# Optimization experiments

Hardware: AMD Instinct MI355X
Metric: run time of the kernel (lower is better)

The kernel has to match this reference:

```python
import jax, jax.numpy as jnp
import numpy as np

TEMPERATURE = 0.2
HYPER_GAMMA = 0.5
EPS = 1e-12  # torch F.normalize / cosine_similarity eps guard (1e-12 / 1e-8)

def setup_inputs() -> dict:
    key = jax.random.key(0)
    k1, k2 = jax.random.split(key)
    B, D = 4096, 1024
    return {
        "emb_i": jax.random.normal(k1, (B, D), dtype=jnp.float32),
        "emb_j": jax.random.normal(k2, (B, D), dtype=jnp.float32),
    }

def _l2_normalize(x, eps=EPS):
    n = jnp.sqrt(jnp.sum(x * x, axis=1, keepdims=True))
    return x / jnp.maximum(n, eps)

def reference(emb_i, emb_j):
    B = emb_i.shape[0]
    z_i = _l2_normalize(emb_i)
    z_j = _l2_normalize(emb_j)
    # cosine similarity of unit vectors == dot product; sim[a, b] = <z_j[a], z_i[b]>
    sim = jnp.einsum('ad,bd->ab', z_j, z_i)  # [B, B]
    sim_positive = jnp.diagonal(sim)
    positives_exp = jnp.exp(-sim_positive + TEMPERATURE)
    neg_mask = 1.0 - jnp.eye(B, dtype=sim.dtype)
    negatives_exp = neg_mask * jnp.exp(sim - TEMPERATURE)
    positives_sum = jnp.sum(jnp.log1p(positives_exp)) / B
    negatives_sum = jnp.sum(jnp.log1p(negatives_exp)) / (B * (B - 1))
    return HYPER_GAMMA * positives_sum + (1.0 - HYPER_GAMMA) * negatives_sum
```

## Files before the change

### kernel.cpp

```cpp
#include <hip/hip_runtime.h>
#include <math.h>

#define B_ROWS 4096
#define D_DIM  1024
static constexpr float TEMP = 0.2f;

typedef __attribute__((ext_vector_type(8))) short bf16x8;
typedef __attribute__((ext_vector_type(4))) float f32x4;

__device__ inline unsigned short f2bf(float f) {
    unsigned int u = __float_as_uint(f);
    u += 0x7fffu + ((u >> 16) & 1u);
    return (unsigned short)(u >> 16);
}

__device__ inline void gload_lds16(const unsigned short* g, unsigned short* l) {
    __builtin_amdgcn_global_load_lds(
        (const __attribute__((address_space(1))) unsigned int*)g,
        (__attribute__((address_space(3))) unsigned int*)l,
        16, 0, 0);
}


__global__ void init_acc_kernel(float* __restrict__ w) {
    w[0] = 0.0f;
    w[1] = 0.0f;
}

__global__ __launch_bounds__(256) void norm_cast_kernel(
        const float* __restrict__ emb_i, const float* __restrict__ emb_j,
        unsigned short* __restrict__ Zi, unsigned short* __restrict__ Zj) {
    const int row = blockIdx.x;
    const float* src;
    unsigned short* dst;
    int r;
    if (row < B_ROWS) { src = emb_i; dst = Zi; r = row; }
    else              { src = emb_j; dst = Zj; r = row - B_ROWS; }

    const int t = threadIdx.x;
    const float4* p = (const float4*)(src + (size_t)r * D_DIM);
    float4 v = p[t];
    float s = v.x * v.x + v.y * v.y + v.z * v.z + v.w * v.w;
    #pragma unroll
    for (int off = 32; off > 0; off >>= 1) s += __shfl_down(s, off, 64);
    __shared__ float ls[4];
    __shared__ float invn;
    if ((t & 63) == 0) ls[t >> 6] = s;
    __syncthreads();
    if (t == 0) {
        float tot = ls[0] + ls[1] + ls[2] + ls[3];
        invn = 1.0f / fmaxf(sqrtf(tot), 1e-12f);
    }
    __syncthreads();
    const float inv = invn;
    ushort4 o;
    o.x = f2bf(v.x * inv); o.y = f2bf(v.y * inv);
    o.z = f2bf(v.z * inv); o.w = f2bf(v.w * inv);
    ((ushort4*)(dst + (size_t)r * D_DIM))[t] = o;
}

__global__ __launch_bounds__(256) void simloss_mfma_kernel(
        const unsigned short* __restrict__ Zi,
        const unsigned short* __restrict__ Zj,
        float* __restrict__ w) {
    __shared__ __align__(16) unsigned short lA[128 * 32];
    __shared__ __align__(16) unsigned short lB[128 * 32];
    __shared__ float rn[4], rp[4];

    const int tid  = threadIdx.x;
    const int lane = tid & 63;
    const int wave = tid >> 6;
    const int wy = wave >> 1, wx = wave & 1;

    const int rowBase = blockIdx.y * 128;
    const int colBase = blockIdx.x * 128;

    const int c0 = 2 * wave, c1 = c0 + 1;
    const int srow  = lane >> 2;
    const int skoff = (lane & 3) * 8;
    const unsigned short* gA0 = Zj + (size_t)(rowBase + 16 * c0 + srow) * D_DIM + skoff;
    const unsigned short* gA1 = Zj + (size_t)(rowBase + 16 * c1 + srow) * D_DIM + skoff;
    const unsigned short* gB0 = Zi + (size_t)(colBase + 16 * c0 + srow) * D_DIM + skoff;
    const unsigned short* gB1 = Zi + (size_t)(colBase + 16 * c1 + srow) * D_DIM + skoff;
    unsigned short* sA0 = lA + c0 * 512;
    unsigned short* sA1 = lA + c1 * 512;
    unsigned short* sB0 = lB + c0 * 512;
    unsigned short* sB1 = lB + c1 * 512;

    const unsigned short* fA = lA + ((wy * 64 + (lane & 15)) * 32 + (lane >> 4) * 8);
    const unsigned short* fB = lB + ((wx * 64 + (lane & 15)) * 32 + (lane >> 4) * 8);

    f32x4 acc[4][4];
    #pragma unroll
    for (int i = 0; i < 4; ++i)
        #pragma unroll
        for (int j = 0; j < 4; ++j)
            acc[i][j] = (f32x4){0.f, 0.f, 0.f, 0.f};

    for (int k0 = 0; k0 < D_DIM; k0 += 32) {
        __syncthreads();
        gload_lds16(gA0, sA0);
        gload_lds16(gA1, sA1);
        gload_lds16(gB0, sB0);
        gload_lds16(gB1, sB1);
        gA0 += 32; gA1 += 32; gB0 += 32; gB1 += 32;
        __syncthreads();

        bf16x8 af[4], bf[4];
        #pragma unroll
        for (int i = 0; i < 4; ++i) af[i] = *(const bf16x8*)(fA + i * 16 * 32);
        #pragma unroll
        for (int j = 0; j < 4; ++j) bf[j] = *(const bf16x8*)(fB + j * 16 * 32);
        #pragma unroll
        for (int i = 0; i < 4; ++i)
            #pragma unroll
            for (int j = 0; j < 4; ++j)
                acc[i][j] = __builtin_amdgcn_mfma_f32_16x16x32_bf16(
                    af[i], bf[j], acc[i][j], 0, 0, 0);
    }

    const int cr = (lane >> 4) * 4;
    const int cc = lane & 15;
    float neg = 0.f, pos = 0.f;
    #pragma unroll
    for (int i = 0; i < 4; ++i) {
        const int abase = rowBase + wy * 64 + i * 16 + cr;
        #pragma unroll
        for (int j = 0; j < 4; ++j) {
            const int b = colBase + wx * 64 + j * 16 + cc;
            #pragma unroll
            for (int r = 0; r < 4; ++r) {
                const float x = acc[i][j][r] - TEMP;
                if (abase + r == b) pos += __logf(1.0f + __expf(-x));
                else                neg += __logf(1.0f + __expf(x));
            }
        }
    }

    #pragma unroll
    for (int off = 32; off > 0; off >>= 1) {
        neg += __shfl_down(neg, off, 64);
        pos += __shfl_down(pos, off, 64);
    }
    if (lane == 0) { rn[wave] = neg; rp[wave] = pos; }
    __syncthreads();
    if (tid == 0) {
        atomicAdd(&w[1], rn[0] + rn[1] + rn[2] + rn[3]);
        if (blockIdx.x == blockIdx.y)
            atomicAdd(&w[0], rp[0] + rp[1] + rp[2] + rp[3]);
    }
}

__global__ void finalize_kernel(const float* __restrict__ w, float* __restrict__ out) {
    const float pos = w[0] / (float)B_ROWS;
    const float neg = w[1] / ((float)B_ROWS * (float)(B_ROWS - 1));
    out[0] = 0.5f * pos + 0.5f * neg;
}

extern "C" void kernel_launch(void* const* d_in, const int* in_sizes, int n_in,
                              void* d_out, int out_size, void* d_ws, size_t ws_size,
                              hipStream_t stream) {
    const float* emb_i = (const float*)d_in[0];
    const float* emb_j = (const float*)d_in[1];
    float* w = (float*)d_ws;
    unsigned short* Zi = (unsigned short*)(w + 16);
    unsigned short* Zj = Zi + (size_t)B_ROWS * D_DIM;
    float* out = (float*)d_out;

    init_acc_kernel<<<1, 1, 0, stream>>>(w);
    norm_cast_kernel<<<2 * B_ROWS, 256, 0, stream>>>(emb_i, emb_j, Zi, Zj);
    dim3 grid(B_ROWS / 128, B_ROWS / 128);
    simloss_mfma_kernel<<<grid, 256, 0, stream>>>(Zi, Zj, w);
    finalize_kernel<<<1, 1, 0, stream>>>(w, out);
}
```

Before: 137.5 us.

## Fuse init/finalize kernels, widen K-tile with swizzled LDS, wave-per-row normalize

```diff
diff --git a/kernel.cpp b/kernel.cpp
--- a/kernel.cpp
+++ b/kernel.cpp
@@ -22,73 +22,69 @@
 }
 
 
-__global__ void init_acc_kernel(float* __restrict__ w) {
-    w[0] = 0.0f;
-    w[1] = 0.0f;
-}
-
 __global__ __launch_bounds__(256) void norm_cast_kernel(
         const float* __restrict__ emb_i, const float* __restrict__ emb_j,
-        unsigned short* __restrict__ Zi, unsigned short* __restrict__ Zj) {
-    const int row = blockIdx.x;
-    const float* src;
-    unsigned short* dst;
-    int r;
+        unsigned short* __restrict__ Zi, unsigned short* __restrict__ Zj,
+        float* __restrict__ w) {
+    const int tid = threadIdx.x;
+    if (blockIdx.x == 0 && tid == 0) {
+        w[0] = 0.0f; w[1] = 0.0f;
+        ((unsigned int*)w)[2] = 0u;
+    }
+    const int wave = tid >> 6, lane = tid & 63;
+    const int row = blockIdx.x * 4 + wave;
+    const float* src; unsigned short* dst; int r;
     if (row < B_ROWS) { src = emb_i; dst = Zi; r = row; }
     else              { src = emb_j; dst = Zj; r = row - B_ROWS; }
 
-    const int t = threadIdx.x;
     const float4* p = (const float4*)(src + (size_t)r * D_DIM);
-    float4 v = p[t];
-    float s = v.x * v.x + v.y * v.y + v.z * v.z + v.w * v.w;
+    float4 v0 = p[lane], v1 = p[64 + lane], v2 = p[128 + lane], v3 = p[192 + lane];
+    float s = v0.x*v0.x + v0.y*v0.y + v0.z*v0.z + v0.w*v0.w
+            + v1.x*v1.x + v1.y*v1.y + v1.z*v1.z + v1.w*v1.w
+            + v2.x*v2.x + v2.y*v2.y + v2.z*v2.z + v2.w*v2.w
+            + v3.x*v3.x + v3.y*v3.y + v3.z*v3.z + v3.w*v3.w;
     #pragma unroll
-    for (int off = 32; off > 0; off >>= 1) s += __shfl_down(s, off, 64);
-    __shared__ float ls[4];
-    __shared__ float invn;
-    if ((t & 63) == 0) ls[t >> 6] = s;
-    __syncthreads();
-    if (t == 0) {
-        float tot = ls[0] + ls[1] + ls[2] + ls[3];
-        invn = 1.0f / fmaxf(sqrtf(tot), 1e-12f);
-    }
-    __syncthreads();
-    const float inv = invn;
-    ushort4 o;
-    o.x = f2bf(v.x * inv); o.y = f2bf(v.y * inv);
-    o.z = f2bf(v.z * inv); o.w = f2bf(v.w * inv);
-    ((ushort4*)(dst + (size_t)r * D_DIM))[t] = o;
+    for (int m = 1; m < 64; m <<= 1) s += __shfl_xor(s, m, 64);
+    const float inv = 1.0f / fmaxf(sqrtf(s), 1e-12f);
+
+    ushort4* q = (ushort4*)(dst + (size_t)r * D_DIM);
+    ushort4 o0 = { f2bf(v0.x*inv), f2bf(v0.y*inv), f2bf(v0.z*inv), f2bf(v0.w*inv) };
+    ushort4 o1 = { f2bf(v1.x*inv), f2bf(v1.y*inv), f2bf(v1.z*inv), f2bf(v1.w*inv) };
+    ushort4 o2 = { f2bf(v2.x*inv), f2bf(v2.y*inv), f2bf(v2.z*inv), f2bf(v2.w*inv) };
+    ushort4 o3 = { f2bf(v3.x*inv), f2bf(v3.y*inv), f2bf(v3.z*inv), f2bf(v3.w*inv) };
+    q[lane] = o0; q[64 + lane] = o1; q[128 + lane] = o2; q[192 + lane] = o3;
 }
 
-__global__ __launch_bounds__(256) void simloss_mfma_kernel(
+__global__ __launch_bounds__(256, 4) void simloss_mfma_kernel(
         const unsigned short* __restrict__ Zi,
         const unsigned short* __restrict__ Zj,
-        float* __restrict__ w) {
-    __shared__ __align__(16) unsigned short lA[128 * 32];
-    __shared__ __align__(16) unsigned short lB[128 * 32];
+        float* __restrict__ w, float* __restrict__ out) {
+    __shared__ __align__(16) unsigned short lA[128 * 64];
+    __shared__ __align__(16) unsigned short lB[128 * 64];
     __shared__ float rn[4], rp[4];
 
     const int tid  = threadIdx.x;
     const int lane = tid & 63;
     const int wave = tid >> 6;
     const int wy = wave >> 1, wx = wave & 1;
-
     const int rowBase = blockIdx.y * 128;
     const int colBase = blockIdx.x * 128;
 
-    const int c0 = 2 * wave, c1 = c0 + 1;
-    const int srow  = lane >> 2;
-    const int skoff = (lane & 3) * 8;
-    const unsigned short* gA0 = Zj + (size_t)(rowBase + 16 * c0 + srow) * D_DIM + skoff;
-    const unsigned short* gA1 = Zj + (size_t)(rowBase + 16 * c1 + srow) * D_DIM + skoff;
-    const unsigned short* gB0 = Zi + (size_t)(colBase + 16 * c0 + srow) * D_DIM + skoff;
-    const unsigned short* gB1 = Zi + (size_t)(colBase + 16 * c1 + srow) * D_DIM + skoff;
-    unsigned short* sA0 = lA + c0 * 512;
-    unsigned short* sA1 = lA + c1 * 512;
-    unsigned short* sB0 = lB + c0 * 512;
-    unsigned short* sB1 = lB + c1 * 512;
+    const int lrow = lane >> 3;
+    const int lp   = lane & 7;
+    const int lc   = (lp - lrow) & 7;
+    const unsigned short* gA = Zj + (size_t)(rowBase + wave * 32 + lrow) * D_DIM + lc * 8;
+    const unsigned short* gB = Zi + (size_t)(colBase + wave * 32 + lrow) * D_DIM + lc * 8;
+    unsigned short* sA = lA + wave * 4 * 512;
+    unsigned short* sB = lB + wave * 4 * 512;
 
-    const unsigned short* fA = lA + ((wy * 64 + (lane & 15)) * 32 + (lane >> 4) * 8);
-    const unsigned short* fB = lB + ((wx * 64 + (lane & 15)) * 32 + (lane >> 4) * 8);
+    const int fr = lane & 15;
+    const int p0 = ((lane >> 4) + (lane & 7)) & 7;
+    const int p1 = (p0 + 4) & 7;
+    const unsigned short* fA0 = lA + (wy * 64 + fr) * 64 + p0 * 8;
+    const unsigned short* fA1 = lA + (wy * 64 + fr) * 64 + p1 * 8;
+    const unsigned short* fB0 = lB + (wx * 64 + fr) * 64 + p0 * 8;
+    const unsigned short* fB1 = lB + (wx * 64 + fr) * 64 + p1 * 8;
 
     f32x4 acc[4][4];
     #pragma unroll
@@ -97,26 +93,37 @@
         for (int j = 0; j < 4; ++j)
             acc[i][j] = (f32x4){0.f, 0.f, 0.f, 0.f};
 
-    for (int k0 = 0; k0 < D_DIM; k0 += 32) {
+    for (int k0 = 0; k0 < D_DIM; k0 += 64) {
         __syncthreads();
-        gload_lds16(gA0, sA0);
-        gload_lds16(gA1, sA1);
-        gload_lds16(gB0, sB0);
-        gload_lds16(gB1, sB1);
-        gA0 += 32; gA1 += 32; gB0 += 32; gB1 += 32;
+        #pragma unroll
+        for (int ch = 0; ch < 4; ++ch) {
+            gload_lds16(gA + ch * 8 * D_DIM, sA + ch * 512);
+            gload_lds16(gB + ch * 8 * D_DIM, sB + ch * 512);
+        }
+        gA += 64; gB += 64;
         __syncthreads();
 
-        bf16x8 af[4], bf[4];
+        bf16x8 a[4], b[4];
         #pragma unroll
-        for (int i = 0; i < 4; ++i) af[i] = *(const bf16x8*)(fA + i * 16 * 32);
+        for (int i = 0; i < 4; ++i) a[i] = *(const bf16x8*)(fA0 + i * 1024);
         #pragma unroll
-        for (int j = 0; j < 4; ++j) bf[j] = *(const bf16x8*)(fB + j * 16 * 32);
+        for (int j = 0; j < 4; ++j) b[j] = *(const bf16x8*)(fB0 + j * 1024);
         #pragma unroll
         for (int i = 0; i < 4; ++i)
             #pragma unroll
             for (int j = 0; j < 4; ++j)
                 acc[i][j] = __builtin_amdgcn_mfma_f32_16x16x32_bf16(
-                    af[i], bf[j], acc[i][j], 0, 0, 0);
+                    a[i], b[j], acc[i][j], 0, 0, 0);
+        #pragma unroll
+        for (int i = 0; i < 4; ++i) a[i] = *(const bf16x8*)(fA1 + i * 1024);
+        #pragma unroll
+        for (int j = 0; j < 4; ++j) b[j] = *(const bf16x8*)(fB1 + j * 1024);
+        #pragma unroll
+        for (int i = 0; i < 4; ++i)
+            #pragma unroll
+            for (int j = 0; j < 4; ++j)
+                acc[i][j] = __builtin_amdgcn_mfma_f32_16x16x32_bf16(
+                    a[i], b[j], acc[i][j], 0, 0, 0);
     }
 
     const int cr = (lane >> 4) * 4;
@@ -136,7 +143,6 @@
             }
         }
     }
-
     #pragma unroll
     for (int off = 32; off > 0; off >>= 1) {
         neg += __shfl_down(neg, off, 64);
@@ -148,13 +154,15 @@
         atomicAdd(&w[1], rn[0] + rn[1] + rn[2] + rn[3]);
         if (blockIdx.x == blockIdx.y)
             atomicAdd(&w[0], rp[0] + rp[1] + rp[2] + rp[3]);
+        __threadfence();
+        unsigned int done = atomicAdd(((unsigned int*)w) + 2, 1u);
+        if (done == gridDim.x * gridDim.y - 1) {
+            const float psum = atomicAdd(&w[0], 0.0f);
+            const float nsum = atomicAdd(&w[1], 0.0f);
+            out[0] = 0.5f * (psum / (float)B_ROWS)
+                   + 0.5f * (nsum / ((float)B_ROWS * (float)(B_ROWS - 1)));
+        }
     }
-}
-
-__global__ void finalize_kernel(const float* __restrict__ w, float* __restrict__ out) {
-    const float pos = w[0] / (float)B_ROWS;
-    const float neg = w[1] / ((float)B_ROWS * (float)(B_ROWS - 1));
-    out[0] = 0.5f * pos + 0.5f * neg;
 }
 
 extern "C" void kernel_launch(void* const* d_in, const int* in_sizes, int n_in,
@@ -167,9 +175,7 @@
     unsigned short* Zj = Zi + (size_t)B_ROWS * D_DIM;
     float* out = (float*)d_out;
 
-    init_acc_kernel<<<1, 1, 0, stream>>>(w);
-    norm_cast_kernel<<<2 * B_ROWS, 256, 0, stream>>>(emb_i, emb_j, Zi, Zj);
+    norm_cast_kernel<<<2 * B_ROWS / 4, 256, 0, stream>>>(emb_i, emb_j, Zi, Zj, w);
     dim3 grid(B_ROWS / 128, B_ROWS / 128);
-    simloss_mfma_kernel<<<grid, 256, 0, stream>>>(Zi, Zj, w);
-    finalize_kernel<<<1, 1, 0, stream>>>(w, out);
+    simloss_mfma_kernel<<<grid, 256, 0, stream>>>(Zi, Zj, w, out);
 }
```

Measured after the change: 147.0 us. +6.9%, slower.
